# Kernel tuning notes

Hardware: AMD Instinct MI355X
Metric: run time of the kernel (lower is better)

The kernel has to match this reference:

```python
import jax, jax.numpy as jnp
import numpy as np

NX, NY, NZ = 432, 496, 1
C = 64  # num_bev_features


def setup_inputs() -> dict:
    key = jax.random.key(0)
    k1, k2, k3, k4 = jax.random.split(key, 4)
    P = 128000
    B = 8
    pillar_features = jax.random.normal(k1, (P, C), dtype=jnp.float32)
    coords_b = jax.random.randint(k2, (P,), 0, B, dtype=jnp.int32)
    coords_z = jnp.zeros((P,), dtype=jnp.int32)
    coords_y = jax.random.randint(k3, (P,), 0, NY, dtype=jnp.int32)
    coords_x = jax.random.randint(k4, (P,), 0, NX, dtype=jnp.int32)
    return {
        "pillar_features": pillar_features,
        "coords_b": coords_b,
        "coords_z": coords_z,
        "coords_y": coords_y,
        "coords_x": coords_x,
        "batch_size": 8,
    }


def reference(pillar_features, coords_b, coords_z, coords_y, coords_x, batch_size):
    # flat spatial index exactly as the torch code: z + y*nx + x  (nz == 1 -> z == 0)
    idx = (coords_z + coords_y * NX + coords_x).astype(jnp.int32)  # [P]
    # one fused scatter over all batches: out[b, :, idx] = pillar_features[p, :]
    out = jnp.zeros((batch_size, C, NZ * NY * NX), dtype=pillar_features.dtype)
    out = out.at[coords_b, :, idx].set(pillar_features)
    return out.reshape(batch_size, C * NZ, NY, NX)
```

## Files before the change

### kernel.cpp

```cpp
#include <hip/hip_runtime.h>


#define NXx 432
#define NYy 496
#define SS  (NXx * NYy)
#define CC  64

__global__ void winner_kernel(const int* __restrict__ cb,
                              const int* __restrict__ cz,
                              const int* __restrict__ cy,
                              const int* __restrict__ cx,
                              int* __restrict__ winner, int P) {
    int p = blockIdx.x * blockDim.x + threadIdx.x;
    if (p < P) {
        int idx = cz[p] + cy[p] * NXx + cx[p];
        int slot = cb[p] * SS + idx;
        atomicMax(&winner[slot], p);
    }
}

__global__ void gather_kernel(const float* __restrict__ pf,
                              const int* __restrict__ winner,
                              float* __restrict__ out, int total4) {
    int stride = gridDim.x * blockDim.x;
    for (int i = blockIdx.x * blockDim.x + threadIdx.x; i < total4; i += stride) {
        int flat = i << 2;
        int plane = flat / SS;
        int s     = flat - plane * SS;
        int c     = plane & (CC - 1);
        int b     = plane >> 6;
        const int4 w = *reinterpret_cast<const int4*>(&winner[b * SS + s]);
        float4 o;
        o.x = (w.x >= 0) ? pf[w.x * CC + c] : 0.0f;
        o.y = (w.y >= 0) ? pf[w.y * CC + c] : 0.0f;
        o.z = (w.z >= 0) ? pf[w.z * CC + c] : 0.0f;
        o.w = (w.w >= 0) ? pf[w.w * CC + c] : 0.0f;
        *reinterpret_cast<float4*>(&out[flat]) = o;
    }
}

extern "C" void kernel_launch(void* const* d_in, const int* in_sizes, int n_in,
                              void* d_out, int out_size, void* d_ws, size_t ws_size,
                              hipStream_t stream) {
    const float* pf = (const float*)d_in[0];
    const int* cb   = (const int*)d_in[1];
    const int* cz   = (const int*)d_in[2];
    const int* cy   = (const int*)d_in[3];
    const int* cx   = (const int*)d_in[4];
    float* out      = (float*)d_out;

    const int P = in_sizes[1];
    const int B = out_size / (CC * SS);

    int* winner = (int*)d_ws;
    hipMemsetAsync(winner, 0xFF, (size_t)B * SS * sizeof(int), stream);

    winner_kernel<<<(P + 255) / 256, 256, 0, stream>>>(cb, cz, cy, cx, winner, P);

    const int total4 = out_size >> 2;
    int blocks = (total4 + 255) / 256;
    if (blocks > 2048) blocks = 2048;
    gather_kernel<<<blocks, 256, 0, stream>>>(pf, winner, out, total4);
}
```

Before: 594.4 us.

## Replace per-output gather with per-slot scatter writing all channels

The output pass now gives each thread one spatial slot instead of four consecutive output floats. Each thread reads its winner once, loads the whole 64-channel feature row as float4, and writes one scalar per channel plane, or writes zeros for empty slots. This removes the repeated winner reads and the per-element division across channel planes. In exchange the stores become scalar rather than float4, though they stay coalesced across threads within each channel plane.

```diff
diff --git a/kernel.cpp b/kernel.cpp
--- a/kernel.cpp
+++ b/kernel.cpp
@@ -13,29 +13,34 @@
                               int* __restrict__ winner, int P) {
     int p = blockIdx.x * blockDim.x + threadIdx.x;
     if (p < P) {
-        int idx = cz[p] + cy[p] * NXx + cx[p];
-        int slot = cb[p] * SS + idx;
+        int slot = cb[p] * SS + cz[p] + cy[p] * NXx + cx[p];
         atomicMax(&winner[slot], p);
     }
 }
 
-__global__ void gather_kernel(const float* __restrict__ pf,
-                              const int* __restrict__ winner,
-                              float* __restrict__ out, int total4) {
-    int stride = gridDim.x * blockDim.x;
-    for (int i = blockIdx.x * blockDim.x + threadIdx.x; i < total4; i += stride) {
-        int flat = i << 2;
-        int plane = flat / SS;
-        int s     = flat - plane * SS;
-        int c     = plane & (CC - 1);
-        int b     = plane >> 6;
-        const int4 w = *reinterpret_cast<const int4*>(&winner[b * SS + s]);
-        float4 o;
-        o.x = (w.x >= 0) ? pf[w.x * CC + c] : 0.0f;
-        o.y = (w.y >= 0) ? pf[w.y * CC + c] : 0.0f;
-        o.z = (w.z >= 0) ? pf[w.z * CC + c] : 0.0f;
-        o.w = (w.w >= 0) ? pf[w.w * CC + c] : 0.0f;
-        *reinterpret_cast<float4*>(&out[flat]) = o;
+__global__ void scatter_kernel(const float* __restrict__ pf,
+                               const int* __restrict__ winner,
+                               float* __restrict__ out, int nslots) {
+    int slot = blockIdx.x * blockDim.x + threadIdx.x;
+    if (slot >= nslots) return;
+    int w = winner[slot];
+    int b = slot / SS;
+    int s = slot - b * SS;
+    float* obase = out + (size_t)b * (CC * SS) + s;
+    if (w >= 0) {
+        const float4* prow = reinterpret_cast<const float4*>(pf + (size_t)w * CC);
+        #pragma unroll
+        for (int q = 0; q < CC / 4; ++q) {
+            float4 v = prow[q];
+            obase[(size_t)(4 * q + 0) * SS] = v.x;
+            obase[(size_t)(4 * q + 1) * SS] = v.y;
+            obase[(size_t)(4 * q + 2) * SS] = v.z;
+            obase[(size_t)(4 * q + 3) * SS] = v.w;
+        }
+    } else {
+        #pragma unroll
+        for (int c = 0; c < CC; ++c)
+            obase[(size_t)c * SS] = 0.0f;
     }
 }
 
@@ -49,16 +54,13 @@
     const int* cx   = (const int*)d_in[4];
     float* out      = (float*)d_out;
 
-    const int P = in_sizes[1];
-    const int B = out_size / (CC * SS);
+    const int P      = in_sizes[1];
+    const int nslots = out_size / CC;
 
     int* winner = (int*)d_ws;
-    hipMemsetAsync(winner, 0xFF, (size_t)B * SS * sizeof(int), stream);
+    hipMemsetAsync(winner, 0xFF, (size_t)nslots * sizeof(int), stream);
 
     winner_kernel<<<(P + 255) / 256, 256, 0, stream>>>(cb, cz, cy, cx, winner, P);
 
-    const int total4 = out_size >> 2;
-    int blocks = (total4 + 255) / 256;
-    if (blocks > 2048) blocks = 2048;
-    gather_kernel<<<blocks, 256, 0, stream>>>(pf, winner, out, total4);
+    scatter_kernel<<<(nslots + 255) / 256, 256, 0, stream>>>(pf, winner, out, nslots);
 }
```

Measured after the change: 623.0 us. 4.8% more time.
